# Optimization experiments

Measured on AMD Instinct MI355X. Metric: run time of the kernel, lower is better.

## Reference

```python
import jax, jax.numpy as jnp
import numpy as np

NH, NKV, D = 8, 2, 256
EPS = 1e-6
SCALING = 1.0 / 256.0  # query_rescale_scalar / query_pre_attn_scalar


def _rms(x):
    # Gemma3nRMSNorm with with_scale=False: x / sqrt(mean(x^2) + eps)
    return x * jax.lax.rsqrt(jnp.mean(x * x, axis=-1, keepdims=True) + EPS)


def _rotate_half(x):
    h = x.shape[-1] // 2
    return jnp.concatenate([-x[..., h:], x[..., :h]], axis=-1)


def setup_inputs() -> dict:
    key = jax.random.key(0)
    ks = jax.random.split(key, 5)
    S, H = 4096, 2048
    hidden_states = jax.random.normal(ks[0], (S, H), dtype=jnp.float32)
    # realistic rope cos/sin
    pos = jnp.arange(S, dtype=jnp.float32)
    inv_freq = 1.0 / (10000.0 ** (jnp.arange(0, D, 2, dtype=jnp.float32) / D))
    ang = pos[:, None] * inv_freq[None, :]              # [S, D/2]
    emb = jnp.concatenate([ang, ang], axis=-1)          # [S, D]
    cos = jnp.cos(emb)
    sin = jnp.sin(emb)
    qkv_w = jax.random.normal(ks[1], ((NH + 2 * NKV) * D, H), dtype=jnp.float32) * 0.02
    o_w = jax.random.normal(ks[2], (H, NH * D), dtype=jnp.float32) * 0.02
    return {"hidden_states": hidden_states, "cos": cos, "sin": sin,
            "qkv_w": qkv_w, "o_w": o_w}


def reference(hidden_states, cos, sin, qkv_w, o_w):
    S = hidden_states.shape[0]
    qkv = hidden_states @ qkv_w.T                        # [S, (NH+2NKV)*D]
    q, k, v = jnp.split(qkv, [NH * D, (NH + NKV) * D], axis=-1)
    q = q.reshape(S, NH, D)                              # [S, NH, D]
    k = k.reshape(S, NKV, D)
    v = v.reshape(S, NKV, D)
    # per-head RMSNorm (no learned scale) on q, k, v
    q = _rms(q)
    k = _rms(k)
    v = _rms(v)
    # RoPE on q, k (v untouched)
    c = cos[:, None, :]
    s = sin[:, None, :]
    q = q * c + _rotate_half(q) * s
    k = k * c + _rotate_half(k) * s
    # GQA: expand kv heads to query heads
    rep = NH // NKV
    k = jnp.repeat(k, rep, axis=1)                       # [S, NH, D]
    v = jnp.repeat(v, rep, axis=1)
    scores = jnp.einsum('qhd,khd->hqk', q, k) * SCALING  # [NH, S, S]
    mask = jnp.tril(jnp.ones((S, S), dtype=bool))
    scores = jnp.where(mask[None], scores, jnp.finfo(scores.dtype).min)
    probs = jax.nn.softmax(scores, axis=-1)
    attn = jnp.einsum('hqk,khd->qhd', probs, v)          # [S, NH, D]
    out = attn.reshape(S, NH * D) @ o_w.T                # [S, H]
    return out
```

## Files before the change

kernel.cpp:

```cpp
#include <hip/hip_runtime.h>

#define NHEADS 8
#define NKVH   2
#define HD     256
#define SEQ    4096
#define HID    2048
#define QKVN   3072
#define SCAL   (1.0f/256.0f)
#define NITEMS_SIDE 320

typedef __attribute__((ext_vector_type(8))) __bf16 bf16x8;
typedef __attribute__((ext_vector_type(4))) float  f32x4;

__device__ __forceinline__ unsigned short f2bf(float f) {
  unsigned int u = __builtin_bit_cast(unsigned int, f);
  u += 0x7fffu + ((u >> 16) & 1u);
  return (unsigned short)(u >> 16);
}
__device__ __forceinline__ float bf2f(unsigned short b) {
  return __builtin_bit_cast(float, (unsigned int)b << 16);
}

__device__ __forceinline__ void async_copy16(const void* g, void* l) {
  __builtin_amdgcn_global_load_lds(
      (__attribute__((address_space(1))) void*)(g),
      (__attribute__((address_space(3))) void*)(l), 16, 0, 0);
}

__device__ __forceinline__ int slot_prefix(int b) {
  if (b < 16) return 0;
  if (b < 32) return b - 16;
  if (b < 48) return 16 + 2 * (b - 32);
  return 48 + 3 * (b - 48);
}

__global__ __launch_bounds__(256) void cvt_bf16(const float* __restrict__ in,
                                                unsigned short* __restrict__ out,
                                                int n4) {
  int i = blockIdx.x * 256 + threadIdx.x;
  if (i >= n4) return;
  float4 v = reinterpret_cast<const float4*>(in)[i];
  ushort4 o;
  o.x = f2bf(v.x); o.y = f2bf(v.y); o.z = f2bf(v.z); o.w = f2bf(v.w);
  reinterpret_cast<ushort4*>(out)[i] = o;
}

template <bool OUT_BF16>
__global__ __launch_bounds__(256) void gemm_bt(const unsigned short* __restrict__ A,
                                               const unsigned short* __restrict__ B,
                                               void* __restrict__ C,
                                               int M, int N, int K) {
  __shared__ __align__(16) unsigned short Als[128 * 64];
  __shared__ __align__(16) unsigned short Bls[128 * 64];
  const int t    = threadIdx.x;
  const int lane = t & 63;
  const int wid  = t >> 6;
  const int wr = wid >> 1, wc = wid & 1;
  const int l15 = lane & 15, lg = lane >> 4;
  const int m0 = blockIdx.y * 128, n0 = blockIdx.x * 128;

  f32x4 acc[4][4] = {};

  for (int k0 = 0; k0 < K; k0 += 64) {
    __syncthreads();
#pragma unroll
    for (int i = 0; i < 4; ++i) {
      int c   = i * 256 + t;
      int kc  = c >> 9;
      int row = (c >> 2) & 127;
      int j8  = (c & 3) ^ (row & 3);
      int gcol = k0 + kc * 32 + j8 * 8;
      async_copy16(A + (size_t)(m0 + row) * K + gcol, Als + c * 8);
      async_copy16(B + (size_t)(n0 + row) * K + gcol, Bls + c * 8);
    }
    __syncthreads();
#pragma unroll
    for (int kc = 0; kc < 2; ++kc) {
      bf16x8 af[4], bfr[4];
#pragma unroll
      for (int m = 0; m < 4; ++m) {
        int row   = wr * 64 + m * 16 + l15;
        int chunk = kc * 512 + row * 4 + (lg ^ (row & 3));
        af[m] = *reinterpret_cast<const bf16x8*>(Als + chunk * 8);
      }
#pragma unroll
      for (int n = 0; n < 4; ++n) {
        int row   = wc * 64 + n * 16 + l15;
        int chunk = kc * 512 + row * 4 + (lg ^ (row & 3));
        bfr[n] = *reinterpret_cast<const bf16x8*>(Bls + chunk * 8);
      }
#pragma unroll
      for (int m = 0; m < 4; ++m)
#pragma unroll
        for (int n = 0; n < 4; ++n)
          acc[m][n] = __builtin_amdgcn_mfma_f32_16x16x32_bf16(af[m], bfr[n],
                                                              acc[m][n], 0, 0, 0);
    }
  }

#pragma unroll
  for (int m = 0; m < 4; ++m) {
#pragma unroll
    for (int n = 0; n < 4; ++n) {
      int col = n0 + wc * 64 + n * 16 + l15;
#pragma unroll
      for (int r = 0; r < 4; ++r) {
        int rowg = m0 + wr * 64 + m * 16 + lg * 4 + r;
        if constexpr (OUT_BF16)
          reinterpret_cast<unsigned short*>(C)[(size_t)rowg * N + col] =
              f2bf(acc[m][n][r]);
        else
          reinterpret_cast<float*>(C)[(size_t)rowg * N + col] = acc[m][n][r];
      }
    }
  }
}

__global__ __launch_bounds__(256) void postproc(const unsigned short* __restrict__ qkv,
                                                const float* __restrict__ cosb,
                                                const float* __restrict__ sinb,
                                                unsigned short* __restrict__ q,
                                                unsigned short* __restrict__ k,
                                                unsigned short* __restrict__ vt) {
  const int wid = threadIdx.x >> 6, lane = threadIdx.x & 63;
  const int task = blockIdx.x * 4 + wid;
  const int s = task / 12, comp = task % 12;

  ushort4 raw = reinterpret_cast<const ushort4*>(qkv + (size_t)task * 256)[lane];
  float x0 = bf2f(raw.x), x1 = bf2f(raw.y), x2 = bf2f(raw.z), x3 = bf2f(raw.w);

  float ss = x0 * x0 + x1 * x1 + x2 * x2 + x3 * x3;
#pragma unroll
  for (int m = 1; m < 64; m <<= 1) ss += __shfl_xor(ss, m);
  float inv = rsqrtf(ss * (1.0f / 256.0f) + 1e-6f);
  x0 *= inv; x1 *= inv; x2 *= inv; x3 *= inv;

  if (comp < 10) {
    float4 c  = reinterpret_cast<const float4*>(cosb + (size_t)s * 256)[lane];
    float4 sn = reinterpret_cast<const float4*>(sinb + (size_t)s * 256)[lane];
    float p0 = __shfl_xor(x0, 32), p1 = __shfl_xor(x1, 32);
    float p2 = __shfl_xor(x2, 32), p3 = __shfl_xor(x3, 32);
    float sg = (lane < 32) ? -1.0f : 1.0f;
    x0 = x0 * c.x + sg * p0 * sn.x;
    x1 = x1 * c.y + sg * p1 * sn.y;
    x2 = x2 * c.z + sg * p2 * sn.z;
    x3 = x3 * c.w + sg * p3 * sn.w;
  }

  if (comp < 8) {
    ushort4 o;
    o.x = f2bf(x0 * SCAL); o.y = f2bf(x1 * SCAL);
    o.z = f2bf(x2 * SCAL); o.w = f2bf(x3 * SCAL);
    reinterpret_cast<ushort4*>(q + ((size_t)s * NHEADS + comp) * 256)[lane] = o;
  } else if (comp < 10) {
    ushort4 o;
    o.x = f2bf(x0); o.y = f2bf(x1); o.z = f2bf(x2); o.w = f2bf(x3);
    reinterpret_cast<ushort4*>(k + ((size_t)(comp - 8) * SEQ + s) * 256)[lane] = o;
  } else {
    size_t base = (size_t)(comp - 10) * 1048576 + (size_t)(s >> 5) * 8192 +
                  (size_t)((s >> 3) & 3) * 2048 + (s & 7);
    int d0 = lane * 4;
    vt[base + (size_t)(d0 + 0) * 8] = f2bf(x0);
    vt[base + (size_t)(d0 + 1) * 8] = f2bf(x1);
    vt[base + (size_t)(d0 + 2) * 8] = f2bf(x2);
    vt[base + (size_t)(d0 + 3) * 8] = f2bf(x3);
  }
}

__global__ __launch_bounds__(256, 2) void flash(const unsigned short* __restrict__ q,
                                                const unsigned short* __restrict__ k,
                                                const unsigned short* __restrict__ vtg,
                                                unsigned short* __restrict__ attn,
                                                unsigned short* __restrict__ opart,
                                                float* __restrict__ ml0,
                                                float* __restrict__ mlp,
                                                int* __restrict__ ticket) {
  extern __shared__ __align__(16) unsigned short lds[];
  unsigned short* Kls = lds;
  unsigned short* Vls = lds + 16384;
  unsigned short* Pls = lds + 32768;
  __shared__ int s_item;

  const int tid  = threadIdx.x;
  const int lane = tid & 63, wid = tid >> 6;
  const int l15 = lane & 15, lg = lane >> 4;
  const int side = (blockIdx.x & 7) >> 2;
  const int kvh = side;

  const unsigned short* kbase  = k   + (size_t)kvh * SEQ * 256;
  const unsigned short* vstage = vtg + (size_t)kvh * 1048576;

  for (;;) {
    __syncthreads();
    if (tid == 0) s_item = atomicAdd(ticket + side, 1);
    __syncthreads();
    const int it = s_item;
    if (it >= NITEMS_SIDE) break;

    int b, hpl, j;
    if (it < 128)      { b = 63 - (it >> 3);             int r = it & 7; hpl = r >> 2; j = r & 3; }
    else if (it < 224) { int u = it - 128; b = 47 - u / 6; int r = u % 6; hpl = r / 3;  j = r % 3; }
    else if (it < 288) { int u = it - 224; b = 31 - (u >> 2); int r = u & 3; hpl = r >> 1; j = r & 1; }
    else               { int u = it - 288; b = 15 - (u >> 1); hpl = u & 1; j = 0; }

    const int h0 = kvh * 4 + hpl * 2;
    const int total_t = 2 * b + 2;
    const int t0 = j * 32;
    const int t1 = min(t0 + 32, total_t) - 1;
    const int qb = b * 64 + wid * 16;

    bf16x8 qf[2][8];
#pragma unroll
    for (int g = 0; g < 2; ++g) {
      const unsigned short* qrow =
          q + ((size_t)(qb + l15) * NHEADS + h0 + g) * 256 + lg * 8;
#pragma unroll
      for (int kc = 0; kc < 8; ++kc)
        qf[g][kc] = *reinterpret_cast<const bf16x8*>(qrow + kc * 32);
    }

    f32x4 o[16][2];
#pragma unroll
    for (int i = 0; i < 16; ++i)
#pragma unroll
      for (int g = 0; g < 2; ++g) o[i][g] = f32x4{0.f, 0.f, 0.f, 0.f};
    float mr0 = -1e30f, lr0 = 0.f, mr1 = -1e30f, lr1 = 0.f;

    auto stage = [&](int bb, int t) {
      const int kvb = t * 32;
#pragma unroll
      for (int i = 0; i < 4; ++i) {
        int p = i * 256 + tid;
        int krow = p >> 5, pj = p & 31;
        int jj = (pj & ~7) | ((pj ^ krow) & 7);
        async_copy16(kbase + (size_t)(kvb + krow) * 256 + jj * 8,
                     Kls + bb * 8192 + p * 8);
      }
      const unsigned short* vsrc = vstage + (size_t)t * 8192;
#pragma unroll
      for (int i = 0; i < 4; ++i) {
        int p = i * 256 + tid;
        async_copy16(vsrc + p * 8, Vls + bb * 8192 + p * 8);
      }
    };

    int cur = 0;
    stage(0, t0);
    __syncthreads();

    for (int t = t0; t <= t1; ++t) {
      const int kvb = t * 32;
      if (t + 1 <= t1) stage(cur ^ 1, t + 1);

      if (kvb <= qb + 15) {
        const unsigned short* Kc = Kls + cur * 8192;
        const unsigned short* Vc = Vls + cur * 8192;

        f32x4 s[2][2] = {};
        __builtin_amdgcn_s_setprio(1);
#pragma unroll
        for (int n = 0; n < 2; ++n) {
          const int row = n * 16 + l15;
#pragma unroll
          for (int kc = 0; kc < 8; ++kc) {
            int jj = kc * 4 + lg;
            int pj = (jj & ~7) | ((jj ^ row) & 7);
            bf16x8 kf = *reinterpret_cast<const bf16x8*>(Kc + (row * 32 + pj) * 8);
            s[0][n] = __builtin_amdgcn_mfma_f32_16x16x32_bf16(kf, qf[0][kc], s[0][n], 0, 0, 0);
            s[1][n] = __builtin_amdgcn_mfma_f32_16x16x32_bf16(kf, qf[1][kc], s[1][n], 0, 0, 0);
          }
        }
        __builtin_amdgcn_s_setprio(0);

        if (kvb + 31 > qb) {
#pragma unroll
          for (int n = 0; n < 2; ++n)
#pragma unroll
            for (int r = 0; r < 4; ++r)
              if (kvb + n * 16 + lg * 4 + r > qb + l15) {
                s[0][n][r] = -1e30f;
                s[1][n][r] = -1e30f;
              }
        }

        float pm0 = fmaxf(fmaxf(fmaxf(s[0][0][0], s[0][0][1]), fmaxf(s[0][0][2], s[0][0][3])),
                          fmaxf(fmaxf(s[0][1][0], s[0][1][1]), fmaxf(s[0][1][2], s[0][1][3])));
        float pm1 = fmaxf(fmaxf(fmaxf(s[1][0][0], s[1][0][1]), fmaxf(s[1][0][2], s[1][0][3])),
                          fmaxf(fmaxf(s[1][1][0], s[1][1][1]), fmaxf(s[1][1][2], s[1][1][3])));

        if (__any(fmaxf(pm0 - mr0, pm1 - mr1) > 8.0f)) {
          float q0 = fmaxf(mr0, pm0), q1 = fmaxf(mr1, pm1);
          q0 = fmaxf(q0, __shfl_xor(q0, 16));
          q0 = fmaxf(q0, __shfl_xor(q0, 32));
          q1 = fmaxf(q1, __shfl_xor(q1, 16));
          q1 = fmaxf(q1, __shfl_xor(q1, 32));
          float sc0 = __expf(mr0 - q0), sc1 = __expf(mr1 - q1);
#pragma unroll
          for (int i = 0; i < 16; ++i)
#pragma unroll
            for (int r = 0; r < 4; ++r) {
              o[i][0][r] *= sc0;
              o[i][1][r] *= sc1;
            }
          lr0 *= sc0; lr1 *= sc1;
          mr0 = q0;   mr1 = q1;
        }

#pragma unroll
        for (int n = 0; n < 2; ++n)
#pragma unroll
          for (int r = 0; r < 4; ++r) {
            s[0][n][r] = __expf(s[0][n][r] - mr0);
            s[1][n][r] = __expf(s[1][n][r] - mr1);
          }

        lr0 += ((s[0][0][0] + s[0][0][1]) + (s[0][0][2] + s[0][0][3])) +
               ((s[0][1][0] + s[0][1][1]) + (s[0][1][2] + s[0][1][3]));
        lr1 += ((s[1][0][0] + s[1][0][1]) + (s[1][0][2] + s[1][0][3])) +
               ((s[1][1][0] + s[1][1][1]) + (s[1][1][2] + s[1][1][3]));

#pragma unroll
        for (int g = 0; g < 2; ++g) {
          unsigned short* Pr = Pls + ((wid * 2 + g) * 16 + l15) * 40;
#pragma unroll
          for (int n = 0; n < 2; ++n) {
            ushort4 w;
            w.x = f2bf(s[g][n][0]); w.y = f2bf(s[g][n][1]);
            w.z = f2bf(s[g][n][2]); w.w = f2bf(s[g][n][3]);
            *reinterpret_cast<ushort4*>(Pr + n * 16 + lg * 4) = w;
          }
        }
        asm volatile("s_waitcnt lgkmcnt(0)" ::: "memory");
        __builtin_amdgcn_sched_barrier(0);

        bf16x8 pb0 = *reinterpret_cast<const bf16x8*>(
            Pls + ((wid * 2 + 0) * 16 + l15) * 40 + lg * 8);
        bf16x8 pb1 = *reinterpret_cast<const bf16x8*>(
            Pls + ((wid * 2 + 1) * 16 + l15) * 40 + lg * 8);
        __builtin_amdgcn_s_setprio(1);
#pragma unroll
        for (int dt = 0; dt < 16; ++dt) {
          bf16x8 vf = *reinterpret_cast<const bf16x8*>(
              Vc + ((lg << 8) + dt * 16 + l15) * 8);
          o[dt][0] = __builtin_amdgcn_mfma_f32_16x16x32_bf16(vf, pb0, o[dt][0], 0, 0, 0);
          o[dt][1] = __builtin_amdgcn_mfma_f32_16x16x32_bf16(vf, pb1, o[dt][1], 0, 0, 0);
        }
        __builtin_amdgcn_s_setprio(0);
      }

      __syncthreads();
      cur ^= 1;
    }

    lr0 += __shfl_xor(lr0, 16); lr0 += __shfl_xor(lr0, 32);
    lr1 += __shfl_xor(lr1, 16); lr1 += __shfl_xor(lr1, 32);

    const int qrow = qb + l15;
#pragma unroll
    for (int g = 0; g < 2; ++g) {
      const int head = h0 + g;
      const float mg = g ? mr1 : mr0;
      const float lg_ = g ? lr1 : lr0;
      if (j == 0) {
#pragma unroll
        for (int dt = 0; dt < 16; ++dt) {
          ushort4 w;
          w.x = f2bf(o[dt][g][0]); w.y = f2bf(o[dt][g][1]);
          w.z = f2bf(o[dt][g][2]); w.w = f2bf(o[dt][g][3]);
          *reinterpret_cast<ushort4*>(
              attn + (size_t)qrow * HID + head * 256 + dt * 16 + lg * 4) = w;
        }
        if (lg == 0)
          reinterpret_cast<float2*>(ml0)[head * SEQ + qrow] = float2{mg, lg_};
      } else {
        const int p = slot_prefix(b) + (j - 1);
        const size_t prow = ((size_t)head * 96 + p) * 64 + (qrow & 63);
#pragma unroll
        for (int dt = 0; dt < 16; ++dt) {
          ushort4 w;
          w.x = f2bf(o[dt][g][0]); w.y = f2bf(o[dt][g][1]);
          w.z = f2bf(o[dt][g][2]); w.w = f2bf(o[dt][g][3]);
          *reinterpret_cast<ushort4*>(opart + prow * 256 + dt * 16 + lg * 4) = w;
        }
        if (lg == 0) reinterpret_cast<float2*>(mlp)[prow] = float2{mg, lg_};
      }
    }
  }
}

__global__ __launch_bounds__(256) void merge(const unsigned short* __restrict__ opart,
                                             const float* __restrict__ ml0,
                                             const float* __restrict__ mlp,
                                             unsigned short* __restrict__ attn) {
  const int wid = threadIdx.x >> 6, lane = threadIdx.x & 63;
  const int rid = blockIdx.x * 4 + wid;
  const int h = rid >> 12, s = rid & 4095;
  const int b = s >> 6;
  const int n = (b >> 4) + 1;

  float2 m_l[4];
  m_l[0] = reinterpret_cast<const float2*>(ml0)[rid];
  const int pf = slot_prefix(b);
  size_t prow[4];
  for (int jj = 1; jj < n; ++jj) {
    prow[jj] = ((size_t)h * 96 + pf + jj - 1) * 64 + (s & 63);
    m_l[jj] = reinterpret_cast<const float2*>(mlp)[prow[jj]];
  }

  float M = m_l[0].x;
  for (int jj = 1; jj < n; ++jj) M = fmaxf(M, m_l[jj].x);
  float w[4], L = 0.f;
  for (int jj = 0; jj < n; ++jj) {
    w[jj] = __expf(m_l[jj].x - M);
    L += w[jj] * m_l[jj].y;
  }
  float invL = 1.0f / L;
  for (int jj = 0; jj < n; ++jj) w[jj] *= invL;

  unsigned short* arow = attn + (size_t)s * HID + h * 256;
  ushort4 a = reinterpret_cast<const ushort4*>(arow)[lane];
  float acc0 = w[0] * bf2f(a.x), acc1 = w[0] * bf2f(a.y);
  float acc2 = w[0] * bf2f(a.z), acc3 = w[0] * bf2f(a.w);
  for (int jj = 1; jj < n; ++jj) {
    ushort4 bq = reinterpret_cast<const ushort4*>(opart + prow[jj] * 256)[lane];
    acc0 += w[jj] * bf2f(bq.x); acc1 += w[jj] * bf2f(bq.y);
    acc2 += w[jj] * bf2f(bq.z); acc3 += w[jj] * bf2f(bq.w);
  }
  ushort4 o;
  o.x = f2bf(acc0); o.y = f2bf(acc1); o.z = f2bf(acc2); o.w = f2bf(acc3);
  reinterpret_cast<ushort4*>(arow)[lane] = o;
}

extern "C" void kernel_launch(void* const* d_in, const int* in_sizes, int n_in,
                              void* d_out, int out_size, void* d_ws, size_t ws_size,
                              hipStream_t stream) {
  const float* hs   = (const float*)d_in[0];
  const float* cosb = (const float*)d_in[1];
  const float* sinb = (const float*)d_in[2];
  const float* qkvw = (const float*)d_in[3];
  const float* ow   = (const float*)d_in[4];

  char* ws = (char*)d_ws;
  unsigned short* hs_bf   = (unsigned short*)(ws + 0);
  unsigned short* wqkv_bf = (unsigned short*)(ws + 16777216);
  unsigned short* wo_bf   = (unsigned short*)(ws + 29360128);
  unsigned short* qkv_bf  = (unsigned short*)(ws + 37748736);
  unsigned short* attn_bf = qkv_bf;
  unsigned short* q_bf    = (unsigned short*)(ws + 62914560);
  unsigned short* k_bf    = (unsigned short*)(ws + 79691776);
  unsigned short* vt_bf   = (unsigned short*)(ws + 83886080);
  unsigned short* opart   = (unsigned short*)(ws + 0);
  float*          ml0buf  = (float*)(ws + 25165824);
  float*          mlpbuf  = (float*)(ws + 25427968);
  int*            ticket  = (int*)(ws + 25821184);

  cvt_bf16<<<dim3((SEQ * HID / 4 + 255) / 256), dim3(256), 0, stream>>>(hs, hs_bf, SEQ * HID / 4);
  cvt_bf16<<<dim3((QKVN * HID / 4 + 255) / 256), dim3(256), 0, stream>>>(qkvw, wqkv_bf, QKVN * HID / 4);
  cvt_bf16<<<dim3((HID * HID / 4 + 255) / 256), dim3(256), 0, stream>>>(ow, wo_bf, HID * HID / 4);

  gemm_bt<true><<<dim3(QKVN / 128, SEQ / 128), dim3(256), 0, stream>>>(
      hs_bf, wqkv_bf, qkv_bf, SEQ, QKVN, HID);

  postproc<<<dim3(SEQ * 12 / 4), dim3(256), 0, stream>>>(qkv_bf, cosb, sinb, q_bf, k_bf, vt_bf);

  hipMemsetAsync(ticket, 0, 8, stream);

  flash<<<dim3(512), dim3(256), 75776, stream>>>(q_bf, k_bf, vt_bf, attn_bf,
                                                 opart, ml0buf, mlpbuf, ticket);

  merge<<<dim3(8192), dim3(256), 0, stream>>>(opart, ml0buf, mlpbuf, attn_bf);

  gemm_bt<false><<<dim3(HID / 128, SEQ / 128), dim3(256), 0, stream>>>(
      attn_bf, wo_bf, d_out, SEQ, HID, HID);
}
```

Before: 327.6 us.

## Fuse bf16 conversions, swizzle GEMM blocks per XCD, rebalance flash item schedule

Merges the three fp32-to-bf16 conversion launches into one kernel that writes a contiguous workspace region, removing two launches. It remaps GEMM workgroup indices so consecutive tiles are grouped by `lin & 7`, likely so each XCD works on nearby tiles and shares more data in its L2. It also reorders the flash-attention ticket schedule so the last group interleaves short query blocks of different sizes with split index j, to balance the tail of the persistent work queue. The fused conversion relies on the three bf16 buffers being contiguous in the workspace.

New measurement: 293.3 us. 10.5% less time.

```diff
diff --git a/kernel.cpp b/kernel.cpp
--- a/kernel.cpp
+++ b/kernel.cpp
@@ -34,12 +34,19 @@
   return 48 + 3 * (b - 48);
 }
 
-__global__ __launch_bounds__(256) void cvt_bf16(const float* __restrict__ in,
-                                                unsigned short* __restrict__ out,
-                                                int n4) {
+__global__ __launch_bounds__(256) void cvt_all(const float* __restrict__ a,
+                                               const float* __restrict__ b,
+                                               const float* __restrict__ c,
+                                               unsigned short* __restrict__ out,
+                                               int n1, int n2, int n3) {
   int i = blockIdx.x * 256 + threadIdx.x;
-  if (i >= n4) return;
-  float4 v = reinterpret_cast<const float4*>(in)[i];
+  const float* src;
+  int off;
+  if (i < n1)            { src = a; off = i; }
+  else if (i < n1 + n2)  { src = b; off = i - n1; }
+  else if (i < n1 + n2 + n3) { src = c; off = i - n1 - n2; }
+  else return;
+  float4 v = reinterpret_cast<const float4*>(src)[off];
   ushort4 o;
   o.x = f2bf(v.x); o.y = f2bf(v.y); o.z = f2bf(v.z); o.w = f2bf(v.w);
   reinterpret_cast<ushort4*>(out)[i] = o;
@@ -57,7 +64,11 @@
   const int wid  = t >> 6;
   const int wr = wid >> 1, wc = wid & 1;
   const int l15 = lane & 15, lg = lane >> 4;
-  const int m0 = blockIdx.y * 128, n0 = blockIdx.x * 128;
+
+  const int nwg = gridDim.x * gridDim.y;
+  const int lin = blockIdx.y * gridDim.x + blockIdx.x;
+  const int swz = (lin & 7) * (nwg >> 3) + (lin >> 3);
+  const int m0 = (swz / gridDim.x) * 128, n0 = (swz % gridDim.x) * 128;
 
   f32x4 acc[4][4] = {};
 
@@ -198,10 +209,11 @@
     if (it >= NITEMS_SIDE) break;
 
     int b, hpl, j;
-    if (it < 128)      { b = 63 - (it >> 3);             int r = it & 7; hpl = r >> 2; j = r & 3; }
-    else if (it < 224) { int u = it - 128; b = 47 - u / 6; int r = u % 6; hpl = r / 3;  j = r % 3; }
-    else if (it < 288) { int u = it - 224; b = 31 - (u >> 2); int r = u & 3; hpl = r >> 1; j = r & 1; }
-    else               { int u = it - 288; b = 15 - (u >> 1); hpl = u & 1; j = 0; }
+    if (it < 96)       { b = 63 - it / 6;              int r = it % 6; hpl = r / 3;  j = r % 3; }
+    else if (it < 160) { int u = it - 96;  b = 47 - (u >> 2); int r = u & 3; hpl = r >> 1; j = r & 1; }
+    else if (it < 192) { int u = it - 160; b = 31 - (u >> 1); hpl = u & 1;   j = 0; }
+    else               { int u = it - 192; int m15 = 15 - (u >> 3); int r = u & 7;
+                         int g = r >> 1;   b = g * 16 + m15; hpl = r & 1;    j = g; }
 
     const int h0 = kvh * 4 + hpl * 2;
     const int total_t = 2 * b + 2;
@@ -454,9 +466,9 @@
   float*          mlpbuf  = (float*)(ws + 25427968);
   int*            ticket  = (int*)(ws + 25821184);
 
-  cvt_bf16<<<dim3((SEQ * HID / 4 + 255) / 256), dim3(256), 0, stream>>>(hs, hs_bf, SEQ * HID / 4);
-  cvt_bf16<<<dim3((QKVN * HID / 4 + 255) / 256), dim3(256), 0, stream>>>(qkvw, wqkv_bf, QKVN * HID / 4);
-  cvt_bf16<<<dim3((HID * HID / 4 + 255) / 256), dim3(256), 0, stream>>>(ow, wo_bf, HID * HID / 4);
+  const int n1 = SEQ * HID / 4, n2 = QKVN * HID / 4, n3 = HID * HID / 4;
+  cvt_all<<<dim3((n1 + n2 + n3 + 255) / 256), dim3(256), 0, stream>>>(
+      hs, qkvw, ow, hs_bf, n1, n2, n3);
 
   gemm_bt<true><<<dim3(QKVN / 128, SEQ / 128), dim3(256), 0, stream>>>(
       hs_bf, wqkv_bf, qkv_bf, SEQ, QKVN, HID);
```
